# Optimization experiments

Hardware: AMD Instinct MI355X
Metric: run time of the kernel (lower is better)

The kernel has to match this reference:

```python
import jax, jax.numpy as jnp
import numpy as np

B, IN, H, O, L, G = 4096, 512, 1024, 256, 2, 3


def _lin_init(key, out_dim, in_dim):
    k1, k2 = jax.random.split(key)
    bound = 1.0 / np.sqrt(in_dim)
    w = jax.random.uniform(k1, (out_dim, in_dim), jnp.float32, -bound, bound)
    b = jax.random.uniform(k2, (out_dim,), jnp.float32, -bound, bound)
    return w, b


def setup_inputs() -> dict:
    key = jax.random.key(0)
    ks = jax.random.split(key, 10)
    x = jax.random.normal(ks[0], (B, IN), jnp.float32)
    hidden = jax.random.normal(ks[1], (L, B, H), jnp.float32)
    i2d_w, i2d_b = _lin_init(ks[2], H, IN)
    # stacked GRU params, PyTorch gate order (r, z, n); layer0 input dim == H (after i2d)
    kih = jax.random.split(ks[3], L)
    khh = jax.random.split(ks[4], L)
    gru_w_ih = jnp.stack([_lin_init(kih[l], 3 * H, H)[0] for l in range(L)])
    gru_b_ih = jnp.stack([_lin_init(kih[l], 3 * H, H)[1] for l in range(L)])
    gru_w_hh = jnp.stack([_lin_init(khh[l], 3 * H, H)[0] for l in range(L)])
    gru_b_hh = jnp.stack([_lin_init(khh[l], 3 * H, H)[1] for l in range(L)])
    mu_w, mu_b = _lin_init(ks[5], O * G, H)
    sigma_w, sigma_b = _lin_init(ks[6], O * G, H)
    pi_w, pi_b = _lin_init(ks[7], O * G, H)
    return {"x": x, "hidden": hidden, "i2d_w": i2d_w, "i2d_b": i2d_b,
            "gru_w_ih": gru_w_ih, "gru_w_hh": gru_w_hh,
            "gru_b_ih": gru_b_ih, "gru_b_hh": gru_b_hh,
            "mu_w": mu_w, "mu_b": mu_b, "sigma_w": sigma_w, "sigma_b": sigma_b,
            "pi_w": pi_w, "pi_b": pi_b, "batch_size": B}


def reference(x, hidden, i2d_w, i2d_b, gru_w_ih, gru_w_hh, gru_b_ih, gru_b_hh,
              mu_w, mu_b, sigma_w, sigma_b, pi_w, pi_b, batch_size):
    # input projection + relu
    h1 = jax.nn.relu(x @ i2d_w.T + i2d_b)  # [B, H]
    # single-timestep stacked GRU (PyTorch cell math, gate order r,z,n)
    inp = h1
    new_h = []
    for l in range(hidden.shape[0]):
        h_prev = hidden[l]
        gi = inp @ gru_w_ih[l].T + gru_b_ih[l]   # [B, 3H]
        gh = h_prev @ gru_w_hh[l].T + gru_b_hh[l]
        i_r, i_z, i_n = jnp.split(gi, 3, axis=-1)
        h_r, h_z, h_n = jnp.split(gh, 3, axis=-1)
        r = jax.nn.sigmoid(i_r + h_r)
        z = jax.nn.sigmoid(i_z + h_z)
        n = jnp.tanh(i_n + r * h_n)
        h_new = (1.0 - z) * n + z * h_prev
        new_h.append(h_new)
        inp = h_new
    hidden_out = jnp.stack(new_h)            # [L, B, H]
    h_out = jnp.tanh(inp)                    # [B, H]
    n_g = 3
    o = mu_w.shape[0] // n_g
    pi = jax.nn.softmax((h_out @ pi_w.T + pi_b).reshape(-1, n_g, o), axis=1)
    mu = (h_out @ mu_w.T + mu_b).reshape(-1, n_g, o)
    sig = jax.nn.softplus(h_out @ sigma_w.T + sigma_b).reshape(-1, n_g, o)
    return (mu, sig, pi, hidden_out)
```

## Files before the change

### kernel.cpp

```cpp
#include <hip/hip_runtime.h>
#include <stdint.h>

typedef unsigned short bf16u;
typedef float f32x4 __attribute__((ext_vector_type(4)));
typedef short bf16x8 __attribute__((ext_vector_type(8)));
typedef float f4 __attribute__((ext_vector_type(4)));

#define AS1 __attribute__((address_space(1)))
#define AS3 __attribute__((address_space(3)))

__device__ __forceinline__ float b2f(bf16u u) {
  union { uint32_t i; float f; } v; v.i = ((uint32_t)u) << 16; return v.f;
}
__device__ __forceinline__ uint32_t f2b(float f) {
  union { float f; uint32_t i; } v; v.f = f;
  uint32_t i = v.i;
  return (i + 0x7FFFu + ((i >> 16) & 1u)) >> 16;
}
__device__ __forceinline__ float sigm(float x) { return 1.f / (1.f + __expf(-x)); }
__device__ __forceinline__ float ftanh(float x) {
  float e = __expf(2.f * x);
  return 1.f - 2.f / (e + 1.f);
}

struct CvtSeg { const float* src; char* dst; int blk0; int count; int tobf16; };
struct CvtArgs { CvtSeg s[12]; int nseg; };

__global__ __launch_bounds__(256)
void cvt_multi(CvtArgs a) {
  int b = blockIdx.x, seg = 0;
  while (seg + 1 < a.nseg && b >= a.s[seg + 1].blk0) ++seg;
  const CvtSeg& S = a.s[seg];
  size_t idx = ((size_t)(b - S.blk0) * 2048) + (size_t)threadIdx.x * 8;
  if ((long long)idx >= S.count) return;
  f4 x = *(const f4*)&S.src[idx];
  f4 y = *(const f4*)&S.src[idx + 4];
  if (S.tobf16) {
    uint4 o;
    o.x = (f2b(x[0]) & 0xffffu) | (f2b(x[1]) << 16);
    o.y = (f2b(x[2]) & 0xffffu) | (f2b(x[3]) << 16);
    o.z = (f2b(y[0]) & 0xffffu) | (f2b(y[1]) << 16);
    o.w = (f2b(y[2]) & 0xffffu) | (f2b(y[3]) << 16);
    *(uint4*)((bf16u*)S.dst + idx) = o;
  } else {
    *(f4*)((float*)S.dst + idx) = x;
    *(f4*)((float*)S.dst + idx + 4) = y;
  }
}

struct GemmPtrs {
  const bf16u* A[2];
  const bf16u* W[2];
  const float* bias[2];
  void* C[2];
};

template <int IT, int ACT, int OUTF32>
__global__ __launch_bounds__(256)
void gemm_bt(GemmPtrs p, int N, int K) {
  constexpr int BM = IT * 32;
  __shared__ bf16u sA[BM * 64];
  __shared__ bf16u sB[128 * 64];
  const int z = blockIdx.z;
  const bf16u* __restrict__ A = p.A[z];
  const bf16u* __restrict__ W = p.W[z];
  const float* __restrict__ bias = p.bias[z];

  const int tid  = threadIdx.x;
  const int wave = tid >> 6;
  const int lane = tid & 63;
  const int bn = blockIdx.x, bm = blockIdx.y;

  const int srA = wave * (IT * 8) + (lane >> 3);
  const int srB = wave * 32 + (lane >> 3);
  const int kc  = (lane & 7) ^ ((lane >> 3) & 7);
  const bf16u* ag = A + (size_t)(bm * BM + srA) * K + kc * 8;
  const bf16u* wg = W + (size_t)(bn * 128 + srB) * K + kc * 8;

  const int wm = wave >> 1, wn = wave & 1;
  const int q = lane >> 4, cl = lane & 15;

  int aoff[IT][2], boff[4][2];
#pragma unroll
  for (int i = 0; i < IT; ++i) {
    int m = wm * (IT * 16) + i * 16 + cl;
#pragma unroll
    for (int kk = 0; kk < 2; ++kk)
      aoff[i][kk] = m * 64 + (((q + kk * 4) ^ (m & 7)) * 8);
  }
#pragma unroll
  for (int j = 0; j < 4; ++j) {
    int n = wn * 64 + j * 16 + cl;
#pragma unroll
    for (int kk = 0; kk < 2; ++kk)
      boff[j][kk] = n * 64 + (((q + kk * 4) ^ (n & 7)) * 8);
  }

  f32x4 acc[IT][4] = {};

  for (int k0 = 0; k0 < K; k0 += 64) {
#pragma unroll
    for (int t = 0; t < IT; ++t)
      __builtin_amdgcn_global_load_lds(
          (const AS1 void*)(ag + k0 + (size_t)t * 8 * K),
          (AS3 void*)&sA[wave * IT * 512 + t * 512],
          16, 0, 0);
#pragma unroll
    for (int t = 0; t < 4; ++t)
      __builtin_amdgcn_global_load_lds(
          (const AS1 void*)(wg + k0 + (size_t)t * 8 * K),
          (AS3 void*)&sB[wave * 2048 + t * 512],
          16, 0, 0);
    __syncthreads();
#pragma unroll
    for (int kk = 0; kk < 2; ++kk) {
      bf16x8 af[IT], bfr[4];
#pragma unroll
      for (int i = 0; i < IT; ++i) af[i] = *(const bf16x8*)&sA[aoff[i][kk]];
#pragma unroll
      for (int j = 0; j < 4; ++j) bfr[j] = *(const bf16x8*)&sB[boff[j][kk]];
#pragma unroll
      for (int i = 0; i < IT; ++i)
#pragma unroll
        for (int j = 0; j < 4; ++j)
          acc[i][j] = __builtin_amdgcn_mfma_f32_16x16x32_bf16(af[i], bfr[j], acc[i][j], 0, 0, 0);
    }
    __syncthreads();
  }

  float bv[4];
#pragma unroll
  for (int j = 0; j < 4; ++j)
    bv[j] = bias[bn * 128 + wn * 64 + j * 16 + cl];

  const int row0 = bm * BM + wm * (IT * 16) + q * 4;
  const int col0 = bn * 128 + wn * 64 + cl;
#pragma unroll
  for (int i = 0; i < IT; ++i)
#pragma unroll
    for (int j = 0; j < 4; ++j)
#pragma unroll
      for (int r = 0; r < 4; ++r) {
        float v = acc[i][j][r] + bv[j];
        if (ACT == 1) v = fmaxf(v, 0.f);
        size_t off = (size_t)(row0 + i * 16 + r) * N + (col0 + j * 16);
        if (OUTF32) ((float*)p.C[z])[off] = v;
        else        ((bf16u*)p.C[z])[off] = (bf16u)f2b(v);
      }
}

template <int LAST>
__global__ __launch_bounds__(512)
void gru_fused(const bf16u* __restrict__ inp, const bf16u* __restrict__ hpb,
               const bf16u* __restrict__ wih, const bf16u* __restrict__ whh,
               const float* __restrict__ bih, const float* __restrict__ bhh,
               const float* __restrict__ hpf, float* __restrict__ hid_out,
               bf16u* __restrict__ nxt) {
  constexpr int K = 1024;
  __shared__ bf16u s[640 * 64];
  const int tid  = threadIdx.x;
  const int wave = tid >> 6;
  const int lane = tid & 63;
  const int bn = blockIdx.x, bm = blockIdx.y;
  const int c0 = bn * 64;

  const int rr  = tid >> 3;
  const int kc  = (tid & 7) ^ (rr & 7);
  const int dst0 = rr * 64 + (tid & 7) * 8;
  const bf16u* gI = inp + (size_t)(bm * 128 + rr) * K + kc * 8;
  const bf16u* gH = hpb + (size_t)(bm * 128 + rr) * K + kc * 8;
  const bf16u* gW[6];
#pragma unroll
  for (int p = 0; p < 6; ++p) {
    const bf16u* base = (p < 3) ? wih : whh;
    gW[p] = base + (size_t)((p % 3) * 1024 + c0 + rr) * K + kc * 8;
  }

  const int wm = wave >> 1, wn = wave & 1;
  const int q = lane >> 4, cl = lane & 15;

  int aoff[2][2], boff[2][2];
#pragma unroll
  for (int i = 0; i < 2; ++i) {
    int ai = wm * 32 + i * 16 + cl;
#pragma unroll
    for (int kk = 0; kk < 2; ++kk)
      aoff[i][kk] = ai * 64 + (((q + kk * 4) ^ (ai & 7)) * 8);
  }
#pragma unroll
  for (int j = 0; j < 2; ++j) {
    int br = wn * 32 + j * 16 + cl;
#pragma unroll
    for (int kk = 0; kk < 2; ++kk)
      boff[j][kk] = (256 + br) * 64 + (((q + kk * 4) ^ (br & 7)) * 8);
  }

  f32x4 acc[6][2][2] = {};

  for (int k0 = 0; k0 < K; k0 += 64) {
    __builtin_amdgcn_global_load_lds((const AS1 void*)(gI + k0),
        (AS3 void*)&s[dst0], 16, 0, 0);
    __builtin_amdgcn_global_load_lds((const AS1 void*)(gI + k0 + (size_t)64 * K),
        (AS3 void*)&s[dst0 + 4096], 16, 0, 0);
    __builtin_amdgcn_global_load_lds((const AS1 void*)(gH + k0),
        (AS3 void*)&s[dst0 + 8192], 16, 0, 0);
    __builtin_amdgcn_global_load_lds((const AS1 void*)(gH + k0 + (size_t)64 * K),
        (AS3 void*)&s[dst0 + 12288], 16, 0, 0);
#pragma unroll
    for (int p = 0; p < 6; ++p)
      __builtin_amdgcn_global_load_lds((const AS1 void*)(gW[p] + k0),
          (AS3 void*)&s[dst0 + (4 + p) * 4096], 16, 0, 0);
    __syncthreads();
#pragma unroll
    for (int kk = 0; kk < 2; ++kk) {
      bf16x8 aI[2], aH[2];
#pragma unroll
      for (int i = 0; i < 2; ++i) {
        aI[i] = *(const bf16x8*)&s[aoff[i][kk]];
        aH[i] = *(const bf16x8*)&s[aoff[i][kk] + 8192];
      }
#pragma unroll
      for (int p = 0; p < 6; ++p) {
        bf16x8 b0 = *(const bf16x8*)&s[boff[0][kk] + p * 4096];
        bf16x8 b1 = *(const bf16x8*)&s[boff[1][kk] + p * 4096];
        if (p < 3) {
          acc[p][0][0] = __builtin_amdgcn_mfma_f32_16x16x32_bf16(aI[0], b0, acc[p][0][0], 0, 0, 0);
          acc[p][0][1] = __builtin_amdgcn_mfma_f32_16x16x32_bf16(aI[0], b1, acc[p][0][1], 0, 0, 0);
          acc[p][1][0] = __builtin_amdgcn_mfma_f32_16x16x32_bf16(aI[1], b0, acc[p][1][0], 0, 0, 0);
          acc[p][1][1] = __builtin_amdgcn_mfma_f32_16x16x32_bf16(aI[1], b1, acc[p][1][1], 0, 0, 0);
        } else {
          acc[p][0][0] = __builtin_amdgcn_mfma_f32_16x16x32_bf16(aH[0], b0, acc[p][0][0], 0, 0, 0);
          acc[p][0][1] = __builtin_amdgcn_mfma_f32_16x16x32_bf16(aH[0], b1, acc[p][0][1], 0, 0, 0);
          acc[p][1][0] = __builtin_amdgcn_mfma_f32_16x16x32_bf16(aH[1], b0, acc[p][1][0], 0, 0, 0);
          acc[p][1][1] = __builtin_amdgcn_mfma_f32_16x16x32_bf16(aH[1], b1, acc[p][1][1], 0, 0, 0);
        }
      }
    }
    __syncthreads();
  }

  float bI[3][2], bH[3][2];
#pragma unroll
  for (int g = 0; g < 3; ++g)
#pragma unroll
    for (int j = 0; j < 2; ++j) {
      int col = c0 + wn * 32 + j * 16 + cl;
      bI[g][j] = bih[g * 1024 + col];
      bH[g][j] = bhh[g * 1024 + col];
    }

#pragma unroll
  for (int i = 0; i < 2; ++i)
#pragma unroll
    for (int j = 0; j < 2; ++j)
#pragma unroll
      for (int r_ = 0; r_ < 4; ++r_) {
        int row = bm * 128 + wm * 32 + i * 16 + q * 4 + r_;
        int col = c0 + wn * 32 + j * 16 + cl;
        size_t o = (size_t)row * 1024 + col;
        float vir = acc[0][i][j][r_] + bI[0][j];
        float viz = acc[1][i][j][r_] + bI[1][j];
        float vin = acc[2][i][j][r_] + bI[2][j];
        float vhr = acc[3][i][j][r_] + bH[0][j];
        float vhz = acc[4][i][j][r_] + bH[1][j];
        float vhn = acc[5][i][j][r_] + bH[2][j];
        float rg = sigm(vir + vhr);
        float zg = sigm(viz + vhz);
        float ng = ftanh(vin + rg * vhn);
        float hnew = (1.f - zg) * ng + zg * hpf[o];
        hid_out[o] = hnew;
        nxt[o] = (bf16u)f2b(LAST ? ftanh(hnew) : hnew);
      }
}

__global__ __launch_bounds__(256)
void gemm_heads(const bf16u* __restrict__ A, const bf16u* __restrict__ Wp,
                const float* __restrict__ biasp, float* __restrict__ out_mu,
                float* __restrict__ out_sg, float* __restrict__ rawpi,
                int outHS) {
  constexpr int K = 1024;
  __shared__ bf16u sA[64 * 64];
  __shared__ bf16u sB[128 * 64];
  const int tid  = threadIdx.x;
  const int wave = tid >> 6;
  const int lane = tid & 63;
  const int bn = blockIdx.x, bm = blockIdx.y;

  const int srA = wave * 16 + (lane >> 3);
  const int srB = wave * 32 + (lane >> 3);
  const int kc  = (lane & 7) ^ ((lane >> 3) & 7);
  const bf16u* ag = A + (size_t)(bm * 64 + srA) * K + kc * 8;
  const bf16u* wg = Wp + (size_t)(bn * 128 + srB) * K + kc * 8;

  const int wm = wave >> 1, wn = wave & 1;
  const int q = lane >> 4, cl = lane & 15;

  int aoff[2][2], boff[4][2];
#pragma unroll
  for (int i = 0; i < 2; ++i) {
    int m = wm * 32 + i * 16 + cl;
#pragma unroll
    for (int kk = 0; kk < 2; ++kk)
      aoff[i][kk] = m * 64 + (((q + kk * 4) ^ (m & 7)) * 8);
  }
#pragma unroll
  for (int j = 0; j < 4; ++j) {
    int n = wn * 64 + j * 16 + cl;
#pragma unroll
    for (int kk = 0; kk < 2; ++kk)
      boff[j][kk] = n * 64 + (((q + kk * 4) ^ (n & 7)) * 8);
  }

  f32x4 acc[2][4] = {};
  for (int k0 = 0; k0 < K; k0 += 64) {
#pragma unroll
    for (int t = 0; t < 2; ++t)
      __builtin_amdgcn_global_load_lds(
          (const AS1 void*)(ag + k0 + (size_t)t * 8 * K),
          (AS3 void*)&sA[wave * 1024 + t * 512],
          16, 0, 0);
#pragma unroll
    for (int t = 0; t < 4; ++t)
      __builtin_amdgcn_global_load_lds(
          (const AS1 void*)(wg + k0 + (size_t)t * 8 * K),
          (AS3 void*)&sB[wave * 2048 + t * 512],
          16, 0, 0);
    __syncthreads();
#pragma unroll
    for (int kk = 0; kk < 2; ++kk) {
      bf16x8 af[2], bfr[4];
#pragma unroll
      for (int i = 0; i < 2; ++i) af[i] = *(const bf16x8*)&sA[aoff[i][kk]];
#pragma unroll
      for (int j = 0; j < 4; ++j) bfr[j] = *(const bf16x8*)&sB[boff[j][kk]];
#pragma unroll
      for (int i = 0; i < 2; ++i)
#pragma unroll
        for (int j = 0; j < 4; ++j)
          acc[i][j] = __builtin_amdgcn_mfma_f32_16x16x32_bf16(af[i], bfr[j], acc[i][j], 0, 0, 0);
    }
    __syncthreads();
  }

  float bv[4];
#pragma unroll
  for (int j = 0; j < 4; ++j)
    bv[j] = biasp[bn * 128 + wn * 64 + j * 16 + cl];

  const int head = bn / 6;
  const int ch0 = (bn % 6) * 128 + wn * 64 + cl;
  const int row0 = bm * 64 + wm * 32 + q * 4;
#pragma unroll
  for (int i = 0; i < 2; ++i)
#pragma unroll
    for (int j = 0; j < 4; ++j)
#pragma unroll
      for (int r = 0; r < 4; ++r) {
        float v = acc[i][j][r] + bv[j];
        size_t off = (size_t)(row0 + i * 16 + r) * 768 + (ch0 + j * 16);
        if (head == 0) out_mu[off] = v;
        else if (head == 1)
          out_sg[off] = fmaxf(v, 0.f) + __logf(1.f + __expf(-fabsf(v)));
        else rawpi[off] = v;
      }
}

__global__ __launch_bounds__(256)
void pi_softmax(const float* __restrict__ rawpi, float* __restrict__ out) {
  int t = blockIdx.x * 256 + threadIdx.x;
  int b = t >> 6;
  int o4 = (t & 63) << 2;
  size_t rb = (size_t)b * 768 + o4;
  f4 pi0 = *(const f4*)&rawpi[rb];
  f4 pi1 = *(const f4*)&rawpi[rb + 256];
  f4 pi2 = *(const f4*)&rawpi[rb + 512];
  f4 e0v, e1v, e2v;
#pragma unroll
  for (int c = 0; c < 4; ++c) {
    float m = fmaxf(fmaxf(pi0[c], pi1[c]), pi2[c]);
    float e0 = __expf(pi0[c] - m), e1 = __expf(pi1[c] - m), e2 = __expf(pi2[c] - m);
    float s = 1.f / (e0 + e1 + e2);
    e0v[c] = e0 * s; e1v[c] = e1 * s; e2v[c] = e2 * s;
  }
  *(f4*)&out[rb]       = e0v;
  *(f4*)&out[rb + 256] = e1v;
  *(f4*)&out[rb + 512] = e2v;
}

extern "C" void kernel_launch(void* const* d_in, const int* in_sizes, int n_in,
                              void* d_out, int out_size, void* d_ws, size_t ws_size,
                              hipStream_t stream) {
  const float* x      = (const float*)d_in[0];
  const float* hidden = (const float*)d_in[1];
  const float* i2d_w  = (const float*)d_in[2];
  const float* i2d_b  = (const float*)d_in[3];
  const float* w_ih   = (const float*)d_in[4];
  const float* w_hh   = (const float*)d_in[5];
  const float* b_ih   = (const float*)d_in[6];
  const float* b_hh   = (const float*)d_in[7];
  const float* mu_w   = (const float*)d_in[8];
  const float* mu_b   = (const float*)d_in[9];
  const float* sg_w   = (const float*)d_in[10];
  const float* sg_b   = (const float*)d_in[11];
  const float* pi_w   = (const float*)d_in[12];
  const float* pi_b   = (const float*)d_in[13];
  float* out = (float*)d_out;

  const size_t BH = 4194304;
  const int HS = 3145728;
  float* hid_base = out + (size_t)3 * HS;

  dim3 blk(256, 1, 1);

  bf16u* wb_i2d = (bf16u*)d_ws;
  bf16u* wb_ih  = wb_i2d + 524288;
  bf16u* wb_hh  = wb_ih + 6291456;
  bf16u* wb_hd  = wb_hh + 6291456;
  float* biasp  = (float*)((char*)d_ws + 30932992);
  const size_t wbytes = 30942208;

  {
    CvtArgs a{};
    int nb = 0;
    auto seg = [&](const float* s, void* d, int count, int tobf) {
      a.s[a.nseg++] = {s, (char*)d, nb, count, tobf};
      nb += (count + 2047) / 2048;
    };
    seg(i2d_w, wb_i2d, 524288, 1);
    seg(w_ih,  wb_ih, 6291456, 1);
    seg(w_hh,  wb_hh, 6291456, 1);
    seg(mu_w,  wb_hd, 786432, 1);
    seg(sg_w,  wb_hd + 786432, 786432, 1);
    seg(pi_w,  wb_hd + 1572864, 786432, 1);
    seg(mu_b,  biasp, 768, 0);
    seg(sg_b,  biasp + 768, 768, 0);
    seg(pi_b,  biasp + 1536, 768, 0);
    cvt_multi<<<dim3(nb), blk, 0, stream>>>(a);
  }

  int Bc = 4096;
  while (wbytes + (size_t)Bc * 12288 > ws_size && Bc > 256) Bc >>= 1;
  const int nchunk = 4096 / Bc;

  char* cbase = (char*)d_ws + wbytes;
  bf16u* ws0  = (bf16u*)cbase;
  bf16u* xb   = (bf16u*)(cbase + (size_t)Bc * 2048);
  bf16u* hb0  = (bf16u*)(cbase + (size_t)Bc * 3072);
  bf16u* hb1  = (bf16u*)(cbase + (size_t)Bc * 5120);
  bf16u* nxt0 = (bf16u*)(cbase + (size_t)Bc * 7168);
  float* rawpi = (float*)(cbase + (size_t)Bc * 9216);

  for (int c = 0; c < nchunk; ++c) {
    const size_t off = (size_t)c * Bc;
    const float* h0_c = hidden + off * 1024;
    const float* h1_c = hidden + BH + off * 1024;

    {
      CvtArgs a{};
      int nb = 0;
      auto seg = [&](const float* s, void* d, int count) {
        a.s[a.nseg++] = {s, (char*)d, nb, count, 1};
        nb += (count + 2047) / 2048;
      };
      seg(x + off * 512, xb, Bc * 512);
      seg(h0_c, hb0, Bc * 1024);
      seg(h1_c, hb1, Bc * 1024);
      cvt_multi<<<dim3(nb), blk, 0, stream>>>(a);
    }

    {
      GemmPtrs p{};
      p.A[0] = xb; p.W[0] = wb_i2d; p.bias[0] = i2d_b; p.C[0] = ws0;
      gemm_bt<2, 1, 0><<<dim3(8, Bc / 64, 1), blk, 0, stream>>>(p, 1024, 512);
    }
    gru_fused<0><<<dim3(16, Bc / 128), dim3(512, 1, 1), 0, stream>>>(
        ws0, hb0, wb_ih, wb_hh, b_ih, b_hh, h0_c,
        hid_base + off * 1024, nxt0);
    gru_fused<1><<<dim3(16, Bc / 128), dim3(512, 1, 1), 0, stream>>>(
        nxt0, hb1, wb_ih + 3145728, wb_hh + 3145728, b_ih + 3072, b_hh + 3072,
        h1_c, hid_base + BH + off * 1024, ws0);
    gemm_heads<<<dim3(18, Bc / 64, 1), blk, 0, stream>>>(
        ws0, wb_hd, biasp, out + off * 768, out + HS + off * 768, rawpi, HS);
    pi_softmax<<<dim3(Bc / 4), blk, 0, stream>>>(rawpi, out + 2 * (size_t)HS + off * 768);
  }
}
```

Baseline: 368.0 us.

## Fuse fp32-to-bf16 activation conversion into GEMMs and softmax into heads kernel

Removes the per-chunk conversion kernel by having the i2d GEMM and the GRU kernels read fp32 x and hidden state directly, converting to bf16 in registers before writing to LDS. The pi head is restructured so each block computes all three mixture components for 64 outputs and applies the softmax in the epilogue, which removes the raw-pi buffer and the separate softmax kernel. Launches and intermediate global traffic go down. In exchange the GEMM loops do register-staged fp32 loads with conversion instead of async global-to-LDS copies, and the pi-head blocks carry a larger B tile than the other head blocks.

```diff
diff --git a/kernel.cpp b/kernel.cpp
--- a/kernel.cpp
+++ b/kernel.cpp
@@ -21,6 +21,14 @@
 __device__ __forceinline__ float ftanh(float x) {
   float e = __expf(2.f * x);
   return 1.f - 2.f / (e + 1.f);
+}
+__device__ __forceinline__ uint4 pack8(f4 a, f4 b) {
+  uint4 o;
+  o.x = (f2b(a[0]) & 0xffffu) | (f2b(a[1]) << 16);
+  o.y = (f2b(a[2]) & 0xffffu) | (f2b(a[3]) << 16);
+  o.z = (f2b(b[0]) & 0xffffu) | (f2b(b[1]) << 16);
+  o.w = (f2b(b[2]) & 0xffffu) | (f2b(b[3]) << 16);
+  return o;
 }
 
 struct CvtSeg { const float* src; char* dst; int blk0; int count; int tobf16; };
@@ -36,54 +44,36 @@
   f4 x = *(const f4*)&S.src[idx];
   f4 y = *(const f4*)&S.src[idx + 4];
   if (S.tobf16) {
-    uint4 o;
-    o.x = (f2b(x[0]) & 0xffffu) | (f2b(x[1]) << 16);
-    o.y = (f2b(x[2]) & 0xffffu) | (f2b(x[3]) << 16);
-    o.z = (f2b(y[0]) & 0xffffu) | (f2b(y[1]) << 16);
-    o.w = (f2b(y[2]) & 0xffffu) | (f2b(y[3]) << 16);
-    *(uint4*)((bf16u*)S.dst + idx) = o;
+    *(uint4*)((bf16u*)S.dst + idx) = pack8(x, y);
   } else {
     *(f4*)((float*)S.dst + idx) = x;
     *(f4*)((float*)S.dst + idx + 4) = y;
   }
 }
 
-struct GemmPtrs {
-  const bf16u* A[2];
-  const bf16u* W[2];
-  const float* bias[2];
-  void* C[2];
-};
-
-template <int IT, int ACT, int OUTF32>
 __global__ __launch_bounds__(256)
-void gemm_bt(GemmPtrs p, int N, int K) {
-  constexpr int BM = IT * 32;
-  __shared__ bf16u sA[BM * 64];
+void gemm_i2d(const float* __restrict__ xf, const bf16u* __restrict__ W,
+              const float* __restrict__ bias, bf16u* __restrict__ Cout) {
+  constexpr int K = 512, N = 1024;
+  __shared__ bf16u sA[64 * 64];
   __shared__ bf16u sB[128 * 64];
-  const int z = blockIdx.z;
-  const bf16u* __restrict__ A = p.A[z];
-  const bf16u* __restrict__ W = p.W[z];
-  const float* __restrict__ bias = p.bias[z];
-
-  const int tid  = threadIdx.x;
-  const int wave = tid >> 6;
-  const int lane = tid & 63;
+  const int tid = threadIdx.x, wave = tid >> 6, lane = tid & 63;
   const int bn = blockIdx.x, bm = blockIdx.y;
 
-  const int srA = wave * (IT * 8) + (lane >> 3);
+  const int srA = wave * 16 + (lane >> 3);
   const int srB = wave * 32 + (lane >> 3);
   const int kc  = (lane & 7) ^ ((lane >> 3) & 7);
-  const bf16u* ag = A + (size_t)(bm * BM + srA) * K + kc * 8;
+  const float* gx = xf + (size_t)(bm * 64 + srA) * K + kc * 8;
   const bf16u* wg = W + (size_t)(bn * 128 + srB) * K + kc * 8;
+  const int adst = srA * 64 + (lane & 7) * 8;
 
   const int wm = wave >> 1, wn = wave & 1;
   const int q = lane >> 4, cl = lane & 15;
 
-  int aoff[IT][2], boff[4][2];
-#pragma unroll
-  for (int i = 0; i < IT; ++i) {
-    int m = wm * (IT * 16) + i * 16 + cl;
+  int aoff[2][2], boff[4][2];
+#pragma unroll
+  for (int i = 0; i < 2; ++i) {
+    int m = wm * 32 + i * 16 + cl;
 #pragma unroll
     for (int kk = 0; kk < 2; ++kk)
       aoff[i][kk] = m * 64 + (((q + kk * 4) ^ (m & 7)) * 8);
@@ -96,31 +86,29 @@
       boff[j][kk] = n * 64 + (((q + kk * 4) ^ (n & 7)) * 8);
   }
 
-  f32x4 acc[IT][4] = {};
-
+  f32x4 acc[2][4] = {};
   for (int k0 = 0; k0 < K; k0 += 64) {
-#pragma unroll
-    for (int t = 0; t < IT; ++t)
-      __builtin_amdgcn_global_load_lds(
-          (const AS1 void*)(ag + k0 + (size_t)t * 8 * K),
-          (AS3 void*)&sA[wave * IT * 512 + t * 512],
-          16, 0, 0);
+    f4 a0 = *(const f4*)(gx + k0);
+    f4 a1 = *(const f4*)(gx + k0 + 4);
+    f4 a2 = *(const f4*)(gx + (size_t)8 * K + k0);
+    f4 a3 = *(const f4*)(gx + (size_t)8 * K + k0 + 4);
 #pragma unroll
     for (int t = 0; t < 4; ++t)
       __builtin_amdgcn_global_load_lds(
           (const AS1 void*)(wg + k0 + (size_t)t * 8 * K),
-          (AS3 void*)&sB[wave * 2048 + t * 512],
-          16, 0, 0);
+          (AS3 void*)&sB[wave * 2048 + t * 512], 16, 0, 0);
+    *(uint4*)&sA[adst]       = pack8(a0, a1);
+    *(uint4*)&sA[adst + 512] = pack8(a2, a3);
     __syncthreads();
 #pragma unroll
     for (int kk = 0; kk < 2; ++kk) {
-      bf16x8 af[IT], bfr[4];
-#pragma unroll
-      for (int i = 0; i < IT; ++i) af[i] = *(const bf16x8*)&sA[aoff[i][kk]];
+      bf16x8 af[2], bfr[4];
+#pragma unroll
+      for (int i = 0; i < 2; ++i) af[i] = *(const bf16x8*)&sA[aoff[i][kk]];
 #pragma unroll
       for (int j = 0; j < 4; ++j) bfr[j] = *(const bf16x8*)&sB[boff[j][kk]];
 #pragma unroll
-      for (int i = 0; i < IT; ++i)
+      for (int i = 0; i < 2; ++i)
 #pragma unroll
         for (int j = 0; j < 4; ++j)
           acc[i][j] = __builtin_amdgcn_mfma_f32_16x16x32_bf16(af[i], bfr[j], acc[i][j], 0, 0, 0);
@@ -133,25 +121,22 @@
   for (int j = 0; j < 4; ++j)
     bv[j] = bias[bn * 128 + wn * 64 + j * 16 + cl];
 
-  const int row0 = bm * BM + wm * (IT * 16) + q * 4;
+  const int row0 = bm * 64 + wm * 32 + q * 4;
   const int col0 = bn * 128 + wn * 64 + cl;
 #pragma unroll
-  for (int i = 0; i < IT; ++i)
+  for (int i = 0; i < 2; ++i)
 #pragma unroll
     for (int j = 0; j < 4; ++j)
 #pragma unroll
       for (int r = 0; r < 4; ++r) {
-        float v = acc[i][j][r] + bv[j];
-        if (ACT == 1) v = fmaxf(v, 0.f);
-        size_t off = (size_t)(row0 + i * 16 + r) * N + (col0 + j * 16);
-        if (OUTF32) ((float*)p.C[z])[off] = v;
-        else        ((bf16u*)p.C[z])[off] = (bf16u)f2b(v);
+        float v = fmaxf(acc[i][j][r] + bv[j], 0.f);
+        Cout[(size_t)(row0 + i * 16 + r) * N + (col0 + j * 16)] = (bf16u)f2b(v);
       }
 }
 
 template <int LAST>
 __global__ __launch_bounds__(512)
-void gru_fused(const bf16u* __restrict__ inp, const bf16u* __restrict__ hpb,
+void gru_fused(const bf16u* __restrict__ inp,
                const bf16u* __restrict__ wih, const bf16u* __restrict__ whh,
                const float* __restrict__ bih, const float* __restrict__ bhh,
                const float* __restrict__ hpf, float* __restrict__ hid_out,
@@ -168,7 +153,7 @@
   const int kc  = (tid & 7) ^ (rr & 7);
   const int dst0 = rr * 64 + (tid & 7) * 8;
   const bf16u* gI = inp + (size_t)(bm * 128 + rr) * K + kc * 8;
-  const bf16u* gH = hpb + (size_t)(bm * 128 + rr) * K + kc * 8;
+  const float* gHf = hpf + (size_t)(bm * 128 + rr) * K + kc * 8;
   const bf16u* gW[6];
 #pragma unroll
   for (int p = 0; p < 6; ++p) {
@@ -198,18 +183,20 @@
   f32x4 acc[6][2][2] = {};
 
   for (int k0 = 0; k0 < K; k0 += 64) {
+    f4 h0a = *(const f4*)(gHf + k0);
+    f4 h0b = *(const f4*)(gHf + k0 + 4);
+    f4 h1a = *(const f4*)(gHf + (size_t)64 * K + k0);
+    f4 h1b = *(const f4*)(gHf + (size_t)64 * K + k0 + 4);
     __builtin_amdgcn_global_load_lds((const AS1 void*)(gI + k0),
         (AS3 void*)&s[dst0], 16, 0, 0);
-    __builtin_amdgcn_global_load_lds((const AS1 void*)(gI + k0 + (size_t)64 * K),
+    __builtin_amdgcn_global_load_lds((const AS1 void*)(gI + (size_t)64 * K + k0),
         (AS3 void*)&s[dst0 + 4096], 16, 0, 0);
-    __builtin_amdgcn_global_load_lds((const AS1 void*)(gH + k0),
-        (AS3 void*)&s[dst0 + 8192], 16, 0, 0);
-    __builtin_amdgcn_global_load_lds((const AS1 void*)(gH + k0 + (size_t)64 * K),
-        (AS3 void*)&s[dst0 + 12288], 16, 0, 0);
 #pragma unroll
     for (int p = 0; p < 6; ++p)
       __builtin_amdgcn_global_load_lds((const AS1 void*)(gW[p] + k0),
           (AS3 void*)&s[dst0 + (4 + p) * 4096], 16, 0, 0);
+    *(uint4*)&s[dst0 + 8192]  = pack8(h0a, h0b);
+    *(uint4*)&s[dst0 + 12288] = pack8(h1a, h1b);
     __syncthreads();
 #pragma unroll
     for (int kk = 0; kk < 2; ++kk) {
@@ -274,28 +261,34 @@
 }
 
 __global__ __launch_bounds__(256)
-void gemm_heads(const bf16u* __restrict__ A, const bf16u* __restrict__ Wp,
-                const float* __restrict__ biasp, float* __restrict__ out_mu,
-                float* __restrict__ out_sg, float* __restrict__ rawpi,
-                int outHS) {
+void gemm_heads2(const bf16u* __restrict__ A, const bf16u* __restrict__ Wp,
+                 const float* __restrict__ biasp, float* __restrict__ out_mu,
+                 float* __restrict__ out_sg, float* __restrict__ out_pi) {
   constexpr int K = 1024;
   __shared__ bf16u sA[64 * 64];
-  __shared__ bf16u sB[128 * 64];
-  const int tid  = threadIdx.x;
-  const int wave = tid >> 6;
-  const int lane = tid & 63;
+  __shared__ bf16u sB[192 * 64];
+  const int tid = threadIdx.x, wave = tid >> 6, lane = tid & 63;
   const int bn = blockIdx.x, bm = blockIdx.y;
+  const bool ispi = (bn >= 12);
+  const int o0 = (bn - 12) * 64;
+  const int nbt = ispi ? 6 : 4;
 
   const int srA = wave * 16 + (lane >> 3);
-  const int srB = wave * 32 + (lane >> 3);
   const int kc  = (lane & 7) ^ ((lane >> 3) & 7);
   const bf16u* ag = A + (size_t)(bm * 64 + srA) * K + kc * 8;
-  const bf16u* wg = Wp + (size_t)(bn * 128 + srB) * K + kc * 8;
+  const bf16u* wg[6];
+#pragma unroll
+  for (int t = 0; t < 6; ++t) {
+    int wrow;
+    if (!ispi) wrow = bn * 128 + t * 32 + wave * 8 + (lane >> 3);
+    else       wrow = 1536 + (t >> 1) * 256 + o0 + (t & 1) * 32 + wave * 8 + (lane >> 3);
+    wg[t] = Wp + (size_t)wrow * K + kc * 8;
+  }
 
   const int wm = wave >> 1, wn = wave & 1;
   const int q = lane >> 4, cl = lane & 15;
 
-  int aoff[2][2], boff[4][2];
+  int aoff[2][2], boff[6][2];
 #pragma unroll
   for (int i = 0; i < 2; ++i) {
     int m = wm * 32 + i * 16 + cl;
@@ -304,87 +297,88 @@
       aoff[i][kk] = m * 64 + (((q + kk * 4) ^ (m & 7)) * 8);
   }
 #pragma unroll
-  for (int j = 0; j < 4; ++j) {
-    int n = wn * 64 + j * 16 + cl;
-#pragma unroll
-    for (int kk = 0; kk < 2; ++kk)
-      boff[j][kk] = n * 64 + (((q + kk * 4) ^ (n & 7)) * 8);
-  }
-
-  f32x4 acc[2][4] = {};
+  for (int j = 0; j < 6; ++j) {
+    int l = ispi ? ((j >> 1) * 64 + wn * 32 + (j & 1) * 16 + cl)
+                 : (wn * 64 + (j & 3) * 16 + cl);
+#pragma unroll
+    for (int kk = 0; kk < 2; ++kk)
+      boff[j][kk] = l * 64 + (((q + kk * 4) ^ (l & 7)) * 8);
+  }
+
+  f32x4 acc[2][6] = {};
   for (int k0 = 0; k0 < K; k0 += 64) {
 #pragma unroll
     for (int t = 0; t < 2; ++t)
       __builtin_amdgcn_global_load_lds(
           (const AS1 void*)(ag + k0 + (size_t)t * 8 * K),
-          (AS3 void*)&sA[wave * 1024 + t * 512],
-          16, 0, 0);
-#pragma unroll
-    for (int t = 0; t < 4; ++t)
-      __builtin_amdgcn_global_load_lds(
-          (const AS1 void*)(wg + k0 + (size_t)t * 8 * K),
-          (AS3 void*)&sB[wave * 2048 + t * 512],
-          16, 0, 0);
+          (AS3 void*)&sA[wave * 1024 + t * 512], 16, 0, 0);
+#pragma unroll
+    for (int t = 0; t < 6; ++t)
+      if (t < nbt)
+        __builtin_amdgcn_global_load_lds(
+            (const AS1 void*)(wg[t] + k0),
+            (AS3 void*)&sB[t * 2048 + wave * 512], 16, 0, 0);
     __syncthreads();
 #pragma unroll
     for (int kk = 0; kk < 2; ++kk) {
-      bf16x8 af[2], bfr[4];
+      bf16x8 af[2];
 #pragma unroll
       for (int i = 0; i < 2; ++i) af[i] = *(const bf16x8*)&sA[aoff[i][kk]];
 #pragma unroll
-      for (int j = 0; j < 4; ++j) bfr[j] = *(const bf16x8*)&sB[boff[j][kk]];
-#pragma unroll
-      for (int i = 0; i < 2; ++i)
-#pragma unroll
-        for (int j = 0; j < 4; ++j)
-          acc[i][j] = __builtin_amdgcn_mfma_f32_16x16x32_bf16(af[i], bfr[j], acc[i][j], 0, 0, 0);
+      for (int j = 0; j < 6; ++j) {
+        if (j >= nbt) continue;
+        bf16x8 bf_ = *(const bf16x8*)&sB[boff[j][kk]];
+#pragma unroll
+        for (int i = 0; i < 2; ++i)
+          acc[i][j] = __builtin_amdgcn_mfma_f32_16x16x32_bf16(af[i], bf_, acc[i][j], 0, 0, 0);
+      }
     }
     __syncthreads();
   }
 
-  float bv[4];
-#pragma unroll
-  for (int j = 0; j < 4; ++j)
-    bv[j] = biasp[bn * 128 + wn * 64 + j * 16 + cl];
-
-  const int head = bn / 6;
-  const int ch0 = (bn % 6) * 128 + wn * 64 + cl;
   const int row0 = bm * 64 + wm * 32 + q * 4;
-#pragma unroll
-  for (int i = 0; i < 2; ++i)
+  if (!ispi) {
+    float bv[4];
 #pragma unroll
     for (int j = 0; j < 4; ++j)
-#pragma unroll
-      for (int r = 0; r < 4; ++r) {
-        float v = acc[i][j][r] + bv[j];
-        size_t off = (size_t)(row0 + i * 16 + r) * 768 + (ch0 + j * 16);
-        if (head == 0) out_mu[off] = v;
-        else if (head == 1)
-          out_sg[off] = fmaxf(v, 0.f) + __logf(1.f + __expf(-fabsf(v)));
-        else rawpi[off] = v;
-      }
-}
-
-__global__ __launch_bounds__(256)
-void pi_softmax(const float* __restrict__ rawpi, float* __restrict__ out) {
-  int t = blockIdx.x * 256 + threadIdx.x;
-  int b = t >> 6;
-  int o4 = (t & 63) << 2;
-  size_t rb = (size_t)b * 768 + o4;
-  f4 pi0 = *(const f4*)&rawpi[rb];
-  f4 pi1 = *(const f4*)&rawpi[rb + 256];
-  f4 pi2 = *(const f4*)&rawpi[rb + 512];
-  f4 e0v, e1v, e2v;
-#pragma unroll
-  for (int c = 0; c < 4; ++c) {
-    float m = fmaxf(fmaxf(pi0[c], pi1[c]), pi2[c]);
-    float e0 = __expf(pi0[c] - m), e1 = __expf(pi1[c] - m), e2 = __expf(pi2[c] - m);
-    float s = 1.f / (e0 + e1 + e2);
-    e0v[c] = e0 * s; e1v[c] = e1 * s; e2v[c] = e2 * s;
-  }
-  *(f4*)&out[rb]       = e0v;
-  *(f4*)&out[rb + 256] = e1v;
-  *(f4*)&out[rb + 512] = e2v;
+      bv[j] = biasp[bn * 128 + wn * 64 + j * 16 + cl];
+    const int head = bn / 6;
+    const int ch0 = (bn % 6) * 128 + wn * 64 + cl;
+#pragma unroll
+    for (int i = 0; i < 2; ++i)
+#pragma unroll
+      for (int j = 0; j < 4; ++j)
+#pragma unroll
+        for (int r = 0; r < 4; ++r) {
+          float v = acc[i][j][r] + bv[j];
+          size_t off = (size_t)(row0 + i * 16 + r) * 768 + (ch0 + j * 16);
+          if (head == 0) out_mu[off] = v;
+          else out_sg[off] = fmaxf(v, 0.f) + __logf(1.f + __expf(-fabsf(v)));
+        }
+  } else {
+    float bv[6];
+#pragma unroll
+    for (int j = 0; j < 6; ++j)
+      bv[j] = biasp[1536 + (j >> 1) * 256 + o0 + wn * 32 + (j & 1) * 16 + cl];
+#pragma unroll
+    for (int i = 0; i < 2; ++i)
+#pragma unroll
+      for (int jo = 0; jo < 2; ++jo)
+#pragma unroll
+        for (int r = 0; r < 4; ++r) {
+          float v0 = acc[i][jo][r]     + bv[jo];
+          float v1 = acc[i][2 + jo][r] + bv[2 + jo];
+          float v2 = acc[i][4 + jo][r] + bv[4 + jo];
+          float m = fmaxf(fmaxf(v0, v1), v2);
+          float e0 = __expf(v0 - m), e1 = __expf(v1 - m), e2 = __expf(v2 - m);
+          float sc = 1.f / (e0 + e1 + e2);
+          size_t base = (size_t)(row0 + i * 16 + r) * 768
+                        + (o0 + wn * 32 + jo * 16 + cl);
+          out_pi[base]       = e0 * sc;
+          out_pi[base + 256] = e1 * sc;
+          out_pi[base + 512] = e2 * sc;
+        }
+  }
 }
 
 extern "C" void kernel_launch(void* const* d_in, const int* in_sizes, int n_in,
@@ -439,48 +433,27 @@
   }
 
   int Bc = 4096;
-  while (wbytes + (size_t)Bc * 12288 > ws_size && Bc > 256) Bc >>= 1;
+  while (wbytes + (size_t)Bc * 4096 > ws_size && Bc > 256) Bc >>= 1;
   const int nchunk = 4096 / Bc;
 
   char* cbase = (char*)d_ws + wbytes;
   bf16u* ws0  = (bf16u*)cbase;
-  bf16u* xb   = (bf16u*)(cbase + (size_t)Bc * 2048);
-  bf16u* hb0  = (bf16u*)(cbase + (size_t)Bc * 3072);
-  bf16u* hb1  = (bf16u*)(cbase + (size_t)Bc * 5120);
-  bf16u* nxt0 = (bf16u*)(cbase + (size_t)Bc * 7168);
-  float* rawpi = (float*)(cbase + (size_t)Bc * 9216);
+  bf16u* nxt0 = (bf16u*)(cbase + (size_t)Bc * 2048);
 
   for (int c = 0; c < nchunk; ++c) {
     const size_t off = (size_t)c * Bc;
     const float* h0_c = hidden + off * 1024;
     const float* h1_c = hidden + BH + off * 1024;
 
-    {
-      CvtArgs a{};
-      int nb = 0;
-      auto seg = [&](const float* s, void* d, int count) {
-        a.s[a.nseg++] = {s, (char*)d, nb, count, 1};
-        nb += (count + 2047) / 2048;
-      };
-      seg(x + off * 512, xb, Bc * 512);
-      seg(h0_c, hb0, Bc * 1024);
-      seg(h1_c, hb1, Bc * 1024);
-      cvt_multi<<<dim3(nb), blk, 0, stream>>>(a);
-    }
-
-    {
-      GemmPtrs p{};
-      p.A[0] = xb; p.W[0] = wb_i2d; p.bias[0] = i2d_b; p.C[0] = ws0;
-      gemm_bt<2, 1, 0><<<dim3(8, Bc / 64, 1), blk, 0, stream>>>(p, 1024, 512);
-    }
+    gemm_i2d<<<dim3(8, Bc / 64), blk, 0, stream>>>(
+        x + off * 512, wb_i2d, i2d_b, ws0);
     gru_fused<0><<<dim3(16, Bc / 128), dim3(512, 1, 1), 0, stream>>>(
-        ws0, hb0, wb_ih, wb_hh, b_ih, b_hh, h0_c,
-        hid_base + off * 1024, nxt0);
+        ws0, wb_ih, wb_hh, b_ih, b_hh, h0_c, hid_base + off * 1024, nxt0);
     gru_fused<1><<<dim3(16, Bc / 128), dim3(512, 1, 1), 0, stream>>>(
-        nxt0, hb1, wb_ih + 3145728, wb_hh + 3145728, b_ih + 3072, b_hh + 3072,
+        nxt0, wb_ih + 3145728, wb_hh + 3145728, b_ih + 3072, b_hh + 3072,
         h1_c, hid_base + BH + off * 1024, ws0);
-    gemm_heads<<<dim3(18, Bc / 64, 1), blk, 0, stream>>>(
-        ws0, wb_hd, biasp, out + off * 768, out + HS + off * 768, rawpi, HS);
-    pi_softmax<<<dim3(Bc / 4), blk, 0, stream>>>(rawpi, out + 2 * (size_t)HS + off * 768);
-  }
-}
+    gemm_heads2<<<dim3(16, Bc / 64), blk, 0, stream>>>(
+        ws0, wb_hd, biasp, out + off * 768, out + HS + off * 768,
+        out + 2 * (size_t)HS + off * 768);
+  }
+}
```

Measured after the change: 400.2 us. +8.8%, slower.
